# Optimization experiments

Measured on AMD Instinct MI355X. Metric: run time of the kernel, lower is better.

## Reference

```python
import jax, jax.numpy as jnp
import numpy as np

NUM_HEADS = 12
ALPHA = 4.0
EPS = 1e-6

def safe_pow(x, p):
    # relu(x)**p with grad-safe handling of x<=0 (avoids nan from log(0) in pow grads)
    xp = jnp.where(x > 0, x, 1.0)
    return jnp.where(x > 0, xp ** p, 0.0)

def setup_inputs() -> dict:
    key = jax.random.key(0)
    ks = jax.random.split(key, 9)
    B, N, C = 8, 4096, 768
    Hn, hd, ksz = NUM_HEADS, C // NUM_HEADS, 5
    return {
        "x": jax.random.normal(ks[0], (B, N, C), jnp.float32),
        "Wqg": jax.random.normal(ks[1], (C, 2 * C), jnp.float32) * 0.02,
        "Wkv": jax.random.normal(ks[2], (C, 2 * C), jnp.float32) * 0.02,
        "Wproj": jax.random.normal(ks[3], (C, C), jnp.float32) * 0.02,
        "bproj": jnp.zeros((C,), jnp.float32),
        "dwc_w": jax.random.normal(ks[4], (hd, 1, ksz, ksz), jnp.float32) * 0.05,
        "dwc_b": jnp.zeros((hd,), jnp.float32),
        "power_p": jax.random.normal(ks[5], (1, Hn, 1, hd), jnp.float32) * 0.01,
        "scale_p": jax.random.normal(ks[6], (1, 1, C), jnp.float32) * 0.01,
        "pos_enc": jax.random.normal(ks[7], (1, N, C), jnp.float32) * 0.01,
    }

def reference(x, Wqg, Wkv, Wproj, bproj, dwc_w, dwc_b, power_p, scale_p, pos_enc):
    B, N, C = x.shape
    Hn = NUM_HEADS
    hd = C // Hn
    # q/g projection: [B,N,2C] -> q = [...,0,:], g = [...,1,:]
    qg = (x @ Wqg).reshape(B, N, 2, C)
    q, g = qg[:, :, 0], qg[:, :, 1]
    # k/v projection (sr_ratio == 1)
    kvp = x @ Wkv
    k, v = kvp[..., :C], kvp[..., C:]
    k = k + pos_enc
    scale = jax.nn.softplus(scale_p)            # [1,1,C]
    power = 1.0 + ALPHA * jax.nn.sigmoid(power_p)  # [1,Hn,1,hd]
    q = q / scale
    k = k / scale
    # -> [B,Hn,N,hd]
    q = q.reshape(B, N, Hn, hd).transpose(0, 2, 1, 3)
    k = k.reshape(B, N, Hn, hd).transpose(0, 2, 1, 3)
    v = v.reshape(B, N, Hn, hd).transpose(0, 2, 1, 3)
    q_pos = safe_pow(q, power)
    q_neg = safe_pow(-q, power)
    k_pos = safe_pow(k, power)
    k_neg = safe_pow(-k, power)
    q_sim = jnp.concatenate([q_pos, q_neg], -1)  # [B,Hn,N,2hd]
    q_opp = jnp.concatenate([q_neg, q_pos], -1)
    k_cat = jnp.concatenate([k_pos, k_neg], -1)
    v1, v2 = jnp.split(v, 2, axis=-1)            # [B,Hn,N,hd/2]
    n = N
    inv_n = 1.0 / n
    k_mean = k_cat.mean(axis=2, keepdims=True)   # [B,Hn,1,2hd]
    z_sim = 1.0 / (jnp.einsum('bhnk,bhmk->bhnm', q_sim, k_mean) + EPS)  # [B,Hn,N,1]
    kv1 = jnp.einsum('bhnk,bhnv->bhkv', k_cat, v1) * inv_n
    x_sim = jnp.einsum('bhnk,bhkv->bhnv', q_sim, kv1) * z_sim
    z_opp = 1.0 / (jnp.einsum('bhnk,bhmk->bhnm', q_opp, k_mean) + EPS)
    kv2 = jnp.einsum('bhnk,bhnv->bhkv', k_cat, v2) * inv_n
    x_opp = jnp.einsum('bhnk,bhkv->bhnv', q_opp, kv2) * z_opp
    xa = jnp.concatenate([x_sim, x_opp], -1).transpose(0, 2, 1, 3).reshape(B, N, C)
    # depthwise-conv positional branch on v (head-major channel layout)
    Hs = int(np.sqrt(N))
    v_img = v.reshape(B * Hn, Hs, Hs, hd).transpose(0, 3, 1, 2)  # [B*Hn, hd, Hs, Hs]
    v_conv = jax.lax.conv_general_dilated(
        v_img, dwc_w, (1, 1), 'SAME', feature_group_count=hd,
        dimension_numbers=('NCHW', 'OIHW', 'NCHW')) + dwc_b[None, :, None, None]
    v_pos = v_conv.reshape(B, C, N).transpose(0, 2, 1)  # [B,N,C]
    out = (xa + v_pos) * g
    return out @ Wproj + bproj
```

## Files before the change

kernel.cpp:

```cpp
#include <hip/hip_runtime.h>


typedef _Float16 f16;
typedef __attribute__((ext_vector_type(4))) float f32x4;
typedef __attribute__((ext_vector_type(8))) _Float16 f16x8;
typedef __attribute__((ext_vector_type(4))) _Float16 f16x4;

__device__ __forceinline__ void mfma(f32x4& c, f16x8 a, f16x8 b) {
  c = __builtin_amdgcn_mfma_f32_16x16x32_f16(a, b, c, 0, 0, 0);
}

__device__ __forceinline__ void gload_lds16(const f16* g, f16* l) {
  __builtin_amdgcn_global_load_lds(
      (__attribute__((address_space(1))) void*)g,
      (__attribute__((address_space(3))) void*)l, 16, 0, 0);
}

__device__ __forceinline__ f16x8 relu8(f16x8 v) {
  f16x8 r;
#pragma unroll
  for (int u = 0; u < 8; ++u) r[u] = (v[u] > (f16)0) ? v[u] : (f16)0;
  return r;
}
__device__ __forceinline__ f16x8 nrelu8(f16x8 v) {
  f16x8 r;
#pragma unroll
  for (int u = 0; u < 8; ++u) r[u] = (v[u] < (f16)0) ? (f16)(-v[u]) : (f16)0;
  return r;
}

__global__ void prep_scalars_kernel(const float* __restrict__ scale_p,
                                    const float* __restrict__ power_p,
                                    float* __restrict__ iscale,
                                    float* __restrict__ powr) {
  int c = blockIdx.x * 256 + threadIdx.x;
  if (c < 768) {
    float sp = scale_p[c];
    float s = (sp > 20.f) ? sp : log1pf(__expf(sp));
    iscale[c] = 1.f / s;
    powr[c] = 1.f + 4.f / (1.f + __expf(-power_p[c]));
  }
}

__global__ __launch_bounds__(256) void cast_x_kernel(const float* __restrict__ x,
                                                     f16* __restrict__ xblk) {
  __shared__ f16 tile[128 * 72];
  const int kb = blockIdx.x, mt = blockIdx.y, t = threadIdx.x;
  const float* xp = x + (size_t)mt * 128 * 768 + kb * 64;
#pragma unroll
  for (int it = 0; it < 8; ++it) {
    int idx = it * 256 + t;
    int row = idx >> 4, kc4 = (idx & 15) * 4;
    f32x4 v = *(const f32x4*)(xp + (size_t)row * 768 + kc4);
    f16x4 h;
    h[0] = (f16)v[0]; h[1] = (f16)v[1]; h[2] = (f16)v[2]; h[3] = (f16)v[3];
    *(f16x4*)(tile + row * 72 + kc4) = h;
  }
  __syncthreads();
  f16* op = xblk + (size_t)mt * 98304 + kb * 8192;
#pragma unroll
  for (int it = 0; it < 4; ++it) {
    int c = it * 256 + t;
    int kchunk = c >> 7, m = c & 127;
    f16x4 lo = *(const f16x4*)(tile + m * 72 + kchunk * 8);
    f16x4 hi = *(const f16x4*)(tile + m * 72 + kchunk * 8 + 4);
    *(f16x4*)(op + c * 8) = lo;
    *(f16x4*)(op + c * 8 + 4) = hi;
  }
}

__global__ __launch_bounds__(256) void transpose_w_kernel(const float* __restrict__ W,
                                                          f16* __restrict__ outblk,
                                                          int Cc, int col_off) {
  __shared__ float tile[32][33];
  const int c0 = blockIdx.x * 32, r0 = blockIdx.y * 32, t = threadIdx.x;
#pragma unroll
  for (int it = 0; it < 4; ++it) {
    int rr = it * 8 + (t >> 5), cc = t & 31;
    tile[rr][cc] = W[(size_t)(r0 + rr) * Cc + c0 + cc];
  }
  __syncthreads();
  if (t < 128) {
    int cl = t >> 2, rb = t & 3;
    int cg = col_off + c0 + cl;
    int rg = r0 + rb * 8;
    f16x4 v0, v1;
#pragma unroll
    for (int u = 0; u < 4; ++u) v0[u] = (f16)tile[rb * 8 + u][cl];
#pragma unroll
    for (int u = 0; u < 4; ++u) v1[u] = (f16)tile[rb * 8 + 4 + u][cl];
    size_t base = (size_t)(cg >> 7) * 98304 + (size_t)(rg >> 3) * 1024 +
                  (size_t)(cg & 127) * 8;
    *(f16x4*)(outblk + base) = v0;
    *(f16x4*)(outblk + base + 4) = v1;
  }
}

template <int MODE>
__global__ __launch_bounds__(512) void gemm_kernel(
    const f16* __restrict__ Ablk, const f16* __restrict__ Bblk,
    const float* __restrict__ powr, const float* __restrict__ iscale,
    const float* __restrict__ pos_enc, const float* __restrict__ bproj,
    f16* __restrict__ qpow, f16* __restrict__ gbuf, f16* __restrict__ kpow,
    f16* __restrict__ vt, float* __restrict__ outp) {
  constexpr int NW    = (MODE == 0) ? 4 : 2;
  constexpr int MREP  = (MODE == 0) ? 8 : 4;
  constexpr int BCOLT = (MODE == 0) ? 2 : 1;
  constexpr int A_H   = 16384;
  constexpr int STR   = A_H + BCOLT * 8192;
  extern __shared__ f16 smem[];
  const int t = threadIdx.x;
  const int wid = t >> 6, lane = t & 63;
  const int c16 = lane & 15, q = lane >> 4;
  const int mtile = blockIdx.x, ntile = blockIdx.y;
  const int wm = wid / NW, wn = wid % NW;
  const f16* Ap = Ablk + (size_t)mtile * 196608;
  const f16* Bp = Bblk + (size_t)ntile * (BCOLT * 98304);
  const int ahalf = (MODE == 0) ? wm : (wm >> 1);
  const int rbase = (MODE == 0) ? 0 : (wm & 1) * 64;
  const int bhalf = (MODE == 0) ? (wn >> 1) : 0;
  const int cbase = (MODE == 0) ? (wn & 1) * 64 : wn * 64;

  auto STAGE = [&](int buf, int k0) {
    const size_t gk = (size_t)k0 * 128;
#pragma unroll
    for (int h = 0; h < 2; ++h)
#pragma unroll
      for (int r = 0; r < 2; ++r)
        gload_lds16(Ap + h * 98304 + gk + (size_t)(r * 512 + t) * 8,
                    smem + buf * STR + h * 8192 + (r * 512 + wid * 64) * 8);
#pragma unroll
    for (int h = 0; h < BCOLT; ++h)
#pragma unroll
      for (int r = 0; r < 2; ++r)
        gload_lds16(Bp + h * 98304 + gk + (size_t)(r * 512 + t) * 8,
                    smem + buf * STR + A_H + h * 8192 + (r * 512 + wid * 64) * 8);
  };

  f32x4 acc[MREP][4];
#pragma unroll
  for (int i = 0; i < MREP; ++i)
#pragma unroll
    for (int j = 0; j < 4; ++j) acc[i][j] = (f32x4){0.f, 0.f, 0.f, 0.f};

  STAGE(0, 0);
  STAGE(1, 64);
  if constexpr (MODE == 0) asm volatile("s_waitcnt vmcnt(8)");
  else                     asm volatile("s_waitcnt vmcnt(6)");
  __builtin_amdgcn_sched_barrier(0);
  __builtin_amdgcn_s_barrier();
  __builtin_amdgcn_sched_barrier(0);

  for (int j = 0; j < 12; ++j) {
    const int cur = j & 1;
    const f16* A_ = smem + cur * STR + ahalf * 8192;
    const f16* B_ = smem + cur * STR + A_H + bhalf * 8192;
#pragma unroll
    for (int s2 = 0; s2 < 2; ++s2) {
      f16x8 af[MREP], bf[4];
      const int kc = (s2 * 4 + q) * 1024;
#pragma unroll
      for (int mi = 0; mi < MREP; ++mi)
        af[mi] = *(const f16x8*)(A_ + kc + (rbase + mi * 16 + c16) * 8);
#pragma unroll
      for (int ni = 0; ni < 4; ++ni)
        bf[ni] = *(const f16x8*)(B_ + kc + (cbase + ni * 16 + c16) * 8);
      __builtin_amdgcn_s_setprio(1);
#pragma unroll
      for (int mi = 0; mi < MREP; ++mi)
#pragma unroll
        for (int ni = 0; ni < 4; ++ni) mfma(acc[mi][ni], af[mi], bf[ni]);
      __builtin_amdgcn_s_setprio(0);
    }
    if (j < 11) {
      asm volatile("s_waitcnt lgkmcnt(0)");
      __builtin_amdgcn_sched_barrier(0);
      __builtin_amdgcn_s_barrier();
      __builtin_amdgcn_sched_barrier(0);
      if (j < 10) {
        STAGE(cur, (j + 2) * 64);
        if constexpr (MODE == 0) asm volatile("s_waitcnt vmcnt(8)");
        else                     asm volatile("s_waitcnt vmcnt(6)");
      } else {
        asm volatile("s_waitcnt vmcnt(0)");
      }
      __builtin_amdgcn_sched_barrier(0);
      __builtin_amdgcn_s_barrier();
      __builtin_amdgcn_sched_barrier(0);
    }
  }

  if (MODE == 0) {
    const int sec = ntile / 3;
    const int csb = (ntile - sec * 3) * 256;
    const int b = mtile >> 4;
    const int nim0 = (mtile & 15) * 256;
#pragma unroll
    for (int mi = 0; mi < MREP; ++mi) {
      const int nloc = nim0 + wm * 128 + mi * 16 + q * 4;
#pragma unroll
      for (int ni = 0; ni < 4; ++ni) {
        const int cs = csb + wn * 64 + ni * 16 + c16;
        const int h = cs >> 6, d = cs & 63;
        const int bh = b * 12 + h;
        if (sec == 0) {
          const float p = powr[cs], isc = iscale[cs];
          const size_t qb2 = (size_t)bh * 262144 + (size_t)(nloc >> 7) * 8192;
          const int dpo = (d >> 3) * 1024 + (d & 7);
#pragma unroll
          for (int r2 = 0; r2 < 4; ++r2) {
            float val = acc[mi][ni][r2] * isc;
            float av = fabsf(val);
            float e = (av > 0.f) ? exp2f(p * __log2f(av)) : 0.f;
            float s = (val > 0.f) ? e : ((val < 0.f) ? -e : 0.f);
            int mrow = (nloc + r2) & 127;
            qpow[qb2 + mrow * 8 + dpo] = (f16)s;
          }
        } else if (sec == 1) {
#pragma unroll
          for (int r2 = 0; r2 < 4; ++r2)
            gbuf[((size_t)bh * 4096 + nloc + r2) * 64 + d] = (f16)acc[mi][ni][r2];
        } else if (sec == 2) {
          const float p = powr[cs], isc = iscale[cs];
          f16x4 pk;
#pragma unroll
          for (int r2 = 0; r2 < 4; ++r2) {
            int n = nloc + r2;
            float val = (acc[mi][ni][r2] + pos_enc[(size_t)n * 768 + cs]) * isc;
            float av = fabsf(val);
            float e = (av > 0.f) ? exp2f(p * __log2f(av)) : 0.f;
            pk[r2] = (f16)((val > 0.f) ? e : ((val < 0.f) ? -e : 0.f));
          }
          const size_t kb2 =
              (size_t)bh * 262144 + (size_t)(nloc >> 3) * 512 + (nloc & 7);
          *(f16x4*)(kpow + kb2 + (size_t)d * 8) = pk;
        } else {
          f16x4 vv4;
#pragma unroll
          for (int r2 = 0; r2 < 4; ++r2) vv4[r2] = (f16)acc[mi][ni][r2];
          *(f16x4*)(vt + (size_t)(bh * 64 + d) * 4096 + nloc) = vv4;
        }
      }
    }
  } else {
#pragma unroll
    for (int mi = 0; mi < MREP; ++mi) {
      const int tok0 = mtile * 256 + wm * 64 + mi * 16 + q * 4;
#pragma unroll
      for (int ni = 0; ni < 4; ++ni) {
        const int col = ntile * 128 + wn * 64 + ni * 16 + c16;
        const float bb = bproj[col];
#pragma unroll
        for (int r2 = 0; r2 < 4; ++r2)
          outp[(size_t)(tok0 + r2) * 768 + col] = acc[mi][ni][r2] + bb;
      }
    }
  }
}

__global__ __launch_bounds__(256) void kv_kernel(const f16* __restrict__ kpow,
                                                 const f16* __restrict__ vt,
                                                 float* __restrict__ kvp,
                                                 float* __restrict__ ksp) {
  __shared__ f16 Ks[8192];
  __shared__ f16 Vs[4096];
  __shared__ float rp[256], rn[256];
  const int bh = blockIdx.x, split = blockIdx.y, t = threadIdx.x;
  const int wave = t >> 6, lane = t & 63;
  const int c16 = lane & 15, q = lane >> 4;
  const f16* kb = kpow + (size_t)bh * 262144;
  const f16* vb = vt + (size_t)bh * 64 * 4096;
  f32x4 acc[4][2];
#pragma unroll
  for (int i = 0; i < 4; ++i)
#pragma unroll
    for (int j = 0; j < 2; ++j) acc[i][j] = (f32x4){0.f, 0.f, 0.f, 0.f};
  float sp = 0.f, sn = 0.f;

  const int n_beg = split * 1024, n_end = n_beg + 1024;
  for (int n0 = n_beg; n0 < n_end; n0 += 64) {
    f16x8 kr[2], vr[2];
#pragma unroll
    for (int r = 0; r < 2; ++r)
      kr[r] = *(const f16x8*)(kb + (size_t)n0 * 64 + (size_t)(r * 256 + t) * 8);
#pragma unroll
    for (int r = 0; r < 2; ++r) {
      int cc = r * 256 + t;
      int vv = cc >> 3, nc = cc & 7;
      vr[r] = *(const f16x8*)(vb + (size_t)vv * 4096 + n0 + nc * 8);
    }
#pragma unroll
    for (int r = 0; r < 2; ++r)
#pragma unroll
      for (int u = 0; u < 8; ++u) {
        float f = (float)kr[r][u];
        sp += (f > 0.f) ? f : 0.f;
        sn += (f < 0.f) ? -f : 0.f;
      }
    __syncthreads();
#pragma unroll
    for (int r = 0; r < 2; ++r) {
      int cp = r * 256 + t;
      int nch = cp >> 6, d = cp & 63;
      *(f16x8*)(Ks + (size_t)(nch * 1024 + d * 8)) = relu8(kr[r]);
      *(f16x8*)(Ks + (size_t)(nch * 1024 + (d + 64) * 8)) = nrelu8(kr[r]);
    }
#pragma unroll
    for (int r = 0; r < 2; ++r) {
      int cc = r * 256 + t;
      int vv = cc >> 3, nc = cc & 7;
      *(f16x8*)(Vs + (size_t)(nc * 64 + (vv ^ nc)) * 8) = vr[r];
    }
    __syncthreads();
#pragma unroll
    for (int s = 0; s < 2; ++s) {
      f16x8 af[4], bf2[2];
#pragma unroll
      for (int i = 0; i < 4; ++i) {
        int m = i * 16 + c16, nc2 = s * 4 + q;
        af[i] = *(const f16x8*)(Vs + (nc2 * 64 + (m ^ nc2)) * 8);
      }
#pragma unroll
      for (int j = 0; j < 2; ++j)
        bf2[j] = *(const f16x8*)(Ks + ((s * 4 + q) * 128 + wave * 32 + j * 16 + c16) * 8);
#pragma unroll
      for (int i = 0; i < 4; ++i)
#pragma unroll
        for (int j = 0; j < 2; ++j) mfma(acc[i][j], af[i], bf2[j]);
    }
    __syncthreads();
  }
  float* kvb = kvp + (size_t)(bh * 4 + split) * 8192;
#pragma unroll
  for (int i = 0; i < 4; ++i)
#pragma unroll
    for (int j = 0; j < 2; ++j) {
      int kk = wave * 32 + j * 16 + c16;
      int vv0 = i * 16 + q * 4;
#pragma unroll
      for (int r2 = 0; r2 < 4; ++r2)
        kvb[(size_t)(vv0 + r2) * 128 + kk] = acc[i][j][r2];
    }
  rp[t] = sp; rn[t] = sn;
  __syncthreads();
  if (t < 64) {
    float* ko = ksp + (size_t)(bh * 4 + split) * 128;
    ko[t] = rp[t] + rp[t + 64] + rp[t + 128] + rp[t + 192];
    ko[64 + t] = rn[t] + rn[t + 64] + rn[t + 128] + rn[t + 192];
  }
}

__global__ void bx_kernel(const float* __restrict__ kvp,
                          const float* __restrict__ ksp, f16* __restrict__ bxt) {
  const int bh = blockIdx.x, kk = threadIdx.x;
  const float inv_n = 1.f / 4096.f;
  const float* kv0 = kvp + (size_t)bh * 4 * 8192;
  const float* ks0 = ksp + (size_t)bh * 4 * 128;
  f16* ob = bxt + (size_t)bh * 80 * 128;
  for (int nn = 0; nn < 32; ++nn) {
    float v = kv0[nn * 128 + kk] + kv0[8192 + nn * 128 + kk] +
              kv0[16384 + nn * 128 + kk] + kv0[24576 + nn * 128 + kk];
    ob[nn * 128 + kk] = (f16)(v * inv_n);
  }
  const int kx = kk ^ 64;
  for (int nn = 32; nn < 64; ++nn) {
    float v = kv0[nn * 128 + kx] + kv0[8192 + nn * 128 + kx] +
              kv0[16384 + nn * 128 + kx] + kv0[24576 + nn * 128 + kx];
    ob[nn * 128 + kk] = (f16)(v * inv_n);
  }
  float s0 = ks0[kk] + ks0[128 + kk] + ks0[256 + kk] + ks0[384 + kk];
  ob[64 * 128 + kk] = (f16)(s0 * inv_n);
  float s1 = ks0[kx] + ks0[128 + kx] + ks0[256 + kx] + ks0[384 + kx];
  ob[65 * 128 + kk] = (f16)(s1 * inv_n);
  for (int nn = 66; nn < 80; ++nn) ob[nn * 128 + kk] = (f16)0.f;
}

__global__ __launch_bounds__(256) void conv_kernel(const f16* __restrict__ vt,
                                                   const float* __restrict__ w,
                                                   const float* __restrict__ bias,
                                                   f16* __restrict__ vpos) {
  __shared__ float img[68 * 69];
  const int blk = blockIdx.x;
  const int d = blk & 63, bh = blk >> 6;
  const f16* src = vt + (size_t)(bh * 64 + d) * 4096;
  for (int i = threadIdx.x; i < 68 * 68; i += 256) {
    int yy = i / 68, xx = i - yy * 68;
    int y = yy - 2, x = xx - 2;
    float val = 0.f;
    if (((unsigned)y < 64u) && ((unsigned)x < 64u)) val = (float)src[y * 64 + x];
    img[yy * 69 + xx] = val;
  }
  float wr[25];
#pragma unroll
  for (int k = 0; k < 25; ++k) wr[k] = w[d * 25 + k];
  const float bb = bias[d];
  __syncthreads();
  f16* dst = vpos + (size_t)(bh * 64 + d) * 4096;
  for (int g4 = threadIdx.x; g4 < 1024; g4 += 256) {
    int y = g4 >> 4, x4 = (g4 & 15) * 4;
    float o0 = bb, o1 = bb, o2 = bb, o3 = bb;
#pragma unroll
    for (int ky = 0; ky < 5; ++ky) {
      const float* row = img + (y + ky) * 69 + x4;
      float r[8];
#pragma unroll
      for (int u = 0; u < 8; ++u) r[u] = row[u];
#pragma unroll
      for (int kx = 0; kx < 5; ++kx) {
        float wv = wr[ky * 5 + kx];
        o0 += r[kx] * wv;
        o1 += r[kx + 1] * wv;
        o2 += r[kx + 2] * wv;
        o3 += r[kx + 3] * wv;
      }
    }
    f16x4 st;
    st[0] = (f16)o0; st[1] = (f16)o1; st[2] = (f16)o2; st[3] = (f16)o3;
    *(f16x4*)(dst + y * 64 + x4) = st;
  }
}

__global__ __launch_bounds__(256) void xa_kernel(
    const f16* __restrict__ qpow, const f16* __restrict__ bxt,
    const f16* __restrict__ vpos, const f16* __restrict__ gbuf,
    f16* __restrict__ pre) {
  __shared__ f16 Qs[16384];
  __shared__ f16 Ps[64 * 134];
  __shared__ float zs[256];
  const int nb = blockIdx.x, bh = blockIdx.y;
  const int b = bh / 12, h = bh % 12;
  const int t = threadIdx.x;
  const int wave = t >> 6, lane = t & 63;
  const int c16 = lane & 15, q = lane >> 4;
  const f16* qb = qpow + (size_t)bh * 262144 + (size_t)nb * 8192;
  f16x8 qr[4];
#pragma unroll
  for (int r = 0; r < 4; ++r)
    qr[r] = *(const f16x8*)(qb + (size_t)(r * 256 + t) * 8);
#pragma unroll
  for (int r = 0; r < 4; ++r) {
    int c = r * 256 + t;
    int dch = c >> 7, row = c & 127;
    *(f16x8*)(Qs + (size_t)(dch * 1024 + row * 8)) = relu8(qr[r]);
    *(f16x8*)(Qs + (size_t)((dch + 8) * 1024 + row * 8)) = nrelu8(qr[r]);
  }
  {
    const f16* vpb = vpos + (size_t)bh * 262144 + (size_t)nb * 128;
#pragma unroll
    for (int it = 0; it < 4; ++it) {
      int idx = it * 256 + t;
      int col = idx >> 4, nc = idx & 15;
      f16x8 v = *(const f16x8*)(vpb + (size_t)col * 4096 + nc * 8);
      *(f16x8*)(Ps + col * 134 + nc * 8) = v;
    }
  }
  __syncthreads();
  f32x4 acc[2][5];
#pragma unroll
  for (int i = 0; i < 2; ++i)
#pragma unroll
    for (int j = 0; j < 5; ++j) acc[i][j] = (f32x4){0.f, 0.f, 0.f, 0.f};
  const f16* bx = bxt + (size_t)bh * 80 * 128;
#pragma unroll
  for (int s = 0; s < 4; ++s) {
    f16x8 af[2], bf5[5];
#pragma unroll
    for (int i = 0; i < 2; ++i)
      af[i] = *(const f16x8*)(Qs + ((s * 4 + q) * 1024 + (wave * 32 + i * 16 + c16) * 8));
#pragma unroll
    for (int j = 0; j < 5; ++j)
      bf5[j] = *(const f16x8*)(bx + (size_t)(j * 16 + c16) * 128 + s * 32 + q * 8);
#pragma unroll
    for (int i = 0; i < 2; ++i)
#pragma unroll
      for (int j = 0; j < 5; ++j) mfma(acc[i][j], af[i], bf5[j]);
  }
  if (c16 < 2) {
#pragma unroll
    for (int i = 0; i < 2; ++i) {
      int mloc = wave * 32 + i * 16 + q * 4;
#pragma unroll
      for (int r2 = 0; r2 < 4; ++r2) zs[(mloc + r2) * 2 + c16] = acc[i][4][r2];
    }
  }
  __syncthreads();
#pragma unroll
  for (int i = 0; i < 2; ++i) {
    const int mbase = wave * 32 + i * 16 + q * 4;
#pragma unroll
    for (int j = 0; j < 4; ++j) {
      const int col = j * 16 + c16;
      const int cch = h * 64 + col;
      const int zsel = col >> 5;
#pragma unroll
      for (int r2 = 0; r2 < 4; ++r2) {
        const int mloc = mbase + r2;
        const int n = nb * 128 + mloc;
        const float den = zs[mloc * 2 + zsel];
        const float xav = acc[i][j][r2] / (den + 1e-6f);
        const float vp = (float)Ps[col * 134 + mloc];
        const float gg = (float)gbuf[((size_t)bh * 4096 + n) * 64 + col];
        const int tok = b * 4096 + n;
        pre[(size_t)(tok >> 7) * 98304 + (size_t)(cch >> 3) * 1024 +
            (tok & 127) * 8 + (cch & 7)] = (f16)((xav + vp) * gg);
      }
    }
  }
}

extern "C" void kernel_launch(void* const* d_in, const int* in_sizes, int n_in,
                              void* d_out, int out_size, void* d_ws, size_t ws_size,
                              hipStream_t stream) {
  const float* x       = (const float*)d_in[0];
  const float* Wqg     = (const float*)d_in[1];
  const float* Wkv     = (const float*)d_in[2];
  const float* Wproj   = (const float*)d_in[3];
  const float* bproj   = (const float*)d_in[4];
  const float* dwc_w   = (const float*)d_in[5];
  const float* dwc_b   = (const float*)d_in[6];
  const float* power_p = (const float*)d_in[7];
  const float* scale_p = (const float*)d_in[8];
  const float* pos_enc = (const float*)d_in[9];
  float* outp = (float*)d_out;

  char* ws = (char*)d_ws;
  constexpr size_t o_qpow = 0;
  constexpr size_t o_kpow = 50331648;
  constexpr size_t o_vt   = 100663296;
  constexpr size_t o_gbuf = 150994944;
  constexpr size_t o_xblk = 201326592;
  constexpr size_t o_wta  = 251658240;
  constexpr size_t o_wtp  = 256376832;
  constexpr size_t o_isc  = 257556480;
  constexpr size_t o_pwr  = 257560576;
  constexpr size_t o_bxt  = 257564672;

  f16*   qpow = (f16*)(ws + o_qpow);
  f16*   kpow = (f16*)(ws + o_kpow);
  f16*   vt   = (f16*)(ws + o_vt);
  f16*   gbuf = (f16*)(ws + o_gbuf);
  f16*   xblk = (f16*)(ws + o_xblk);
  f16*   wta  = (f16*)(ws + o_wta);
  f16*   wtp  = (f16*)(ws + o_wtp);
  float* isc  = (float*)(ws + o_isc);
  float* pwr  = (float*)(ws + o_pwr);
  f16*   bxt  = (f16*)(ws + o_bxt);
  float* kvp  = (float*)(ws + o_xblk);
  float* ksp  = (float*)(ws + o_xblk + 12582912);
  f16*   vpos = kpow;
  f16*   pre  = xblk;

  prep_scalars_kernel<<<dim3(3), 256, 0, stream>>>(scale_p, power_p, isc, pwr);
  cast_x_kernel<<<dim3(12, 256), 256, 0, stream>>>(x, xblk);
  transpose_w_kernel<<<dim3(48, 24), 256, 0, stream>>>(Wqg, wta, 1536, 0);
  transpose_w_kernel<<<dim3(48, 24), 256, 0, stream>>>(Wkv, wta, 1536, 1536);
  transpose_w_kernel<<<dim3(24, 24), 256, 0, stream>>>(Wproj, wtp, 768, 0);
  gemm_kernel<0><<<dim3(128, 12), 512, 131072, stream>>>(
      xblk, wta, pwr, isc, pos_enc, nullptr, qpow, gbuf, kpow, vt, nullptr);
  kv_kernel<<<dim3(96, 4), 256, 0, stream>>>(kpow, vt, kvp, ksp);
  bx_kernel<<<96, 128, 0, stream>>>(kvp, ksp, bxt);
  conv_kernel<<<6144, 256, 0, stream>>>(vt, dwc_w, dwc_b, vpos);
  xa_kernel<<<dim3(32, 96), 256, 0, stream>>>(qpow, bxt, vpos, gbuf, pre);
  gemm_kernel<1><<<dim3(128, 6), 512, 98304, stream>>>(
      pre, wtp, nullptr, nullptr, nullptr, bproj, nullptr, nullptr, nullptr,
      nullptr, outp);
}
```

Measured before the change: 611.1 us.

## Interleave global-to-LDS prefetch with MFMA phases in GEMM main loop

The GEMM main loop is restructured into finer phases. Each phase issues a slice of the next tiles' global-to-LDS loads between LDS fragment reads and MFMA bursts. Buffer halves are refilled progressively, one row group at a time, instead of as a whole stage after a barrier. The goal is to hide load latency and avoid the stall at the end of each k-step, at the cost of more barriers per iteration and more delicate vmcnt accounting.

After: 635.1 us. 1.04x slower.

```diff
diff --git a/kernel.cpp b/kernel.cpp
--- a/kernel.cpp
+++ b/kernel.cpp
@@ -121,21 +121,14 @@
   const int bhalf = (MODE == 0) ? (wn >> 1) : 0;
   const int cbase = (MODE == 0) ? (wn & 1) * 64 : wn * 64;
 
-  auto STAGE = [&](int buf, int k0) {
-    const size_t gk = (size_t)k0 * 128;
-#pragma unroll
-    for (int h = 0; h < 2; ++h)
-#pragma unroll
-      for (int r = 0; r < 2; ++r)
-        gload_lds16(Ap + h * 98304 + gk + (size_t)(r * 512 + t) * 8,
-                    smem + buf * STR + h * 8192 + (r * 512 + wid * 64) * 8);
-#pragma unroll
-    for (int h = 0; h < BCOLT; ++h)
-#pragma unroll
-      for (int r = 0; r < 2; ++r)
-        gload_lds16(Bp + h * 98304 + gk + (size_t)(r * 512 + t) * 8,
-                    smem + buf * STR + A_H + h * 8192 + (r * 512 + wid * 64) * 8);
+  auto stageA = [&](int buf, int k0, int h, int r) {
+    gload_lds16(Ap + (size_t)h * 98304 + (size_t)k0 * 128 + (size_t)(r * 512 + t) * 8,
+                smem + buf * STR + h * 8192 + (r * 512 + wid * 64) * 8);
   };
+  auto stageB = [&](int buf, int k0, int h, int r) {
+    gload_lds16(Bp + (size_t)h * 98304 + (size_t)k0 * 128 + (size_t)(r * 512 + t) * 8,
+                smem + buf * STR + A_H + h * 8192 + (r * 512 + wid * 64) * 8);
+  };
 
   f32x4 acc[MREP][4];
 #pragma unroll
@@ -143,50 +136,106 @@
 #pragma unroll
     for (int j = 0; j < 4; ++j) acc[i][j] = (f32x4){0.f, 0.f, 0.f, 0.f};
 
-  STAGE(0, 0);
-  STAGE(1, 64);
-  if constexpr (MODE == 0) asm volatile("s_waitcnt vmcnt(8)");
-  else                     asm volatile("s_waitcnt vmcnt(6)");
+  if constexpr (MODE == 0) {
+    stageA(0, 0, 0, 0); stageA(0, 0, 1, 0); stageB(0, 0, 0, 0); stageB(0, 0, 1, 0);
+    stageA(0, 0, 0, 1); stageA(0, 0, 1, 1); stageB(0, 0, 0, 1); stageB(0, 0, 1, 1);
+    stageA(1, 64, 0, 0); stageA(1, 64, 1, 0); stageB(1, 64, 0, 0); stageB(1, 64, 1, 0);
+    asm volatile("s_waitcnt vmcnt(4)");
+  } else {
+    stageA(0, 0, 0, 0); stageA(0, 0, 1, 0); stageB(0, 0, 0, 0);
+    stageA(0, 0, 0, 1); stageA(0, 0, 1, 1); stageB(0, 0, 0, 1);
+    stageA(1, 64, 0, 0); stageA(1, 64, 1, 0); stageB(1, 64, 0, 0);
+    asm volatile("s_waitcnt vmcnt(3)");
+  }
   __builtin_amdgcn_sched_barrier(0);
   __builtin_amdgcn_s_barrier();
   __builtin_amdgcn_sched_barrier(0);
 
-  for (int j = 0; j < 12; ++j) {
-    const int cur = j & 1;
-    const f16* A_ = smem + cur * STR + ahalf * 8192;
-    const f16* B_ = smem + cur * STR + A_H + bhalf * 8192;
-#pragma unroll
-    for (int s2 = 0; s2 < 2; ++s2) {
-      f16x8 af[MREP], bf[4];
-      const int kc = (s2 * 4 + q) * 1024;
-#pragma unroll
-      for (int mi = 0; mi < MREP; ++mi)
-        af[mi] = *(const f16x8*)(A_ + kc + (rbase + mi * 16 + c16) * 8);
-#pragma unroll
-      for (int ni = 0; ni < 4; ++ni)
-        bf[ni] = *(const f16x8*)(B_ + kc + (cbase + ni * 16 + c16) * 8);
-      __builtin_amdgcn_s_setprio(1);
-#pragma unroll
-      for (int mi = 0; mi < MREP; ++mi)
-#pragma unroll
-        for (int ni = 0; ni < 4; ++ni) mfma(acc[mi][ni], af[mi], bf[ni]);
-      __builtin_amdgcn_s_setprio(0);
-    }
-    if (j < 11) {
-      asm volatile("s_waitcnt lgkmcnt(0)");
-      __builtin_amdgcn_sched_barrier(0);
-      __builtin_amdgcn_s_barrier();
-      __builtin_amdgcn_sched_barrier(0);
-      if (j < 10) {
-        STAGE(cur, (j + 2) * 64);
-        if constexpr (MODE == 0) asm volatile("s_waitcnt vmcnt(8)");
-        else                     asm volatile("s_waitcnt vmcnt(6)");
-      } else {
-        asm volatile("s_waitcnt vmcnt(0)");
-      }
-      __builtin_amdgcn_sched_barrier(0);
-      __builtin_amdgcn_s_barrier();
-      __builtin_amdgcn_sched_barrier(0);
+  if constexpr (MODE == 0) {
+    f16x8 bf[4];
+    for (int j = 0; j < 12; ++j) {
+      const int cur = j & 1;
+      const f16* A_ = smem + cur * STR + ahalf * 8192;
+      const f16* B_ = smem + cur * STR + A_H + bhalf * 8192;
+#pragma unroll
+      for (int ph = 0; ph < 4; ++ph) {
+        const int s2 = ph >> 1, mh = ph & 1;
+        const int kc = (s2 * 4 + q) * 1024;
+        f16x8 af[4];
+#pragma unroll
+        for (int mi = 0; mi < 4; ++mi)
+          af[mi] = *(const f16x8*)(A_ + kc + ((mh * 4 + mi) * 16 + c16) * 8);
+        if (mh == 0) {
+#pragma unroll
+          for (int ni = 0; ni < 4; ++ni)
+            bf[ni] = *(const f16x8*)(B_ + kc + (cbase + ni * 16 + c16) * 8);
+        }
+        if (ph == 0 && j < 11) { stageA(cur ^ 1, (j + 1) * 64, 0, 1); stageA(cur ^ 1, (j + 1) * 64, 1, 1); }
+        if (ph == 1 && j < 11) { stageB(cur ^ 1, (j + 1) * 64, 0, 1); stageB(cur ^ 1, (j + 1) * 64, 1, 1); }
+        if (ph == 2 && j < 10) { stageA(cur, (j + 2) * 64, 0, 0); stageA(cur, (j + 2) * 64, 1, 0); }
+        if (ph == 3 && j < 10) { stageB(cur, (j + 2) * 64, 0, 0); stageB(cur, (j + 2) * 64, 1, 0); }
+        __builtin_amdgcn_sched_barrier(0);
+        __builtin_amdgcn_s_barrier();
+        asm volatile("s_waitcnt lgkmcnt(0)");
+        __builtin_amdgcn_sched_barrier(0);
+        __builtin_amdgcn_s_setprio(1);
+#pragma unroll
+        for (int mi = 0; mi < 4; ++mi)
+#pragma unroll
+          for (int ni = 0; ni < 4; ++ni)
+            mfma(acc[mh * 4 + mi][ni], af[mi], bf[ni]);
+        __builtin_amdgcn_s_setprio(0);
+        if (ph == 3) {
+          if (j < 10)       asm volatile("s_waitcnt vmcnt(4)");
+          else if (j == 10) asm volatile("s_waitcnt vmcnt(0)");
+        }
+        __builtin_amdgcn_sched_barrier(0);
+        __builtin_amdgcn_s_barrier();
+        __builtin_amdgcn_sched_barrier(0);
+      }
+    }
+  } else {
+    for (int j = 0; j < 12; ++j) {
+      const int cur = j & 1;
+      const f16* A_ = smem + cur * STR + ahalf * 8192;
+      const f16* B_ = smem + cur * STR + A_H;
+#pragma unroll
+      for (int ph = 0; ph < 2; ++ph) {
+        const int kc = (ph * 4 + q) * 1024;
+        f16x8 af[4], bf[4];
+#pragma unroll
+        for (int mi = 0; mi < 4; ++mi)
+          af[mi] = *(const f16x8*)(A_ + kc + (rbase + mi * 16 + c16) * 8);
+#pragma unroll
+        for (int ni = 0; ni < 4; ++ni)
+          bf[ni] = *(const f16x8*)(B_ + kc + (cbase + ni * 16 + c16) * 8);
+        if (ph == 0 && j < 11) {
+          stageA(cur ^ 1, (j + 1) * 64, 0, 1); stageA(cur ^ 1, (j + 1) * 64, 1, 1);
+          stageB(cur ^ 1, (j + 1) * 64, 0, 1);
+        }
+        if (ph == 1 && j < 10) {
+          stageA(cur, (j + 2) * 64, 0, 0); stageA(cur, (j + 2) * 64, 1, 0);
+          stageB(cur, (j + 2) * 64, 0, 0);
+        }
+        __builtin_amdgcn_sched_barrier(0);
+        __builtin_amdgcn_s_barrier();
+        asm volatile("s_waitcnt lgkmcnt(0)");
+        __builtin_amdgcn_sched_barrier(0);
+        __builtin_amdgcn_s_setprio(1);
+#pragma unroll
+        for (int mi = 0; mi < 4; ++mi)
+#pragma unroll
+          for (int ni = 0; ni < 4; ++ni)
+            mfma(acc[mi][ni], af[mi], bf[ni]);
+        __builtin_amdgcn_s_setprio(0);
+        if (ph == 1) {
+          if (j < 10)       asm volatile("s_waitcnt vmcnt(3)");
+          else if (j == 10) asm volatile("s_waitcnt vmcnt(0)");
+        }
+        __builtin_amdgcn_sched_barrier(0);
+        __builtin_amdgcn_s_barrier();
+        __builtin_amdgcn_sched_barrier(0);
+      }
     }
   }
 
```

## Shrink GEMM tiles to 128x256 with smaller K-steps for higher occupancy

Applied to the files above, without the earlier changes.

Both GEMM instantiations now use one 128x256 tile with a 32-wide K step, static 48KB LDS double buffer, and launch bounds requesting 4 blocks per CU. The prefetch of the next stage is issued before compute of the current one, with a single barrier per iteration. The grid is swapped so N tiles index x, improving A-tile reuse across neighbouring blocks. The aim is more resident waves to hide latency. The cost is less register reuse per block and more barriers over 24 K iterations.

Result: no change. 617.0 us (+1.0%).

```diff
diff --git a/kernel.cpp b/kernel.cpp
--- a/kernel.cpp
+++ b/kernel.cpp
@@ -97,107 +97,80 @@
 }
 
 template <int MODE>
-__global__ __launch_bounds__(512) void gemm_kernel(
+__global__ __launch_bounds__(512, 4) void gemm_kernel(
     const f16* __restrict__ Ablk, const f16* __restrict__ Bblk,
     const float* __restrict__ powr, const float* __restrict__ iscale,
     const float* __restrict__ pos_enc, const float* __restrict__ bproj,
     f16* __restrict__ qpow, f16* __restrict__ gbuf, f16* __restrict__ kpow,
     f16* __restrict__ vt, float* __restrict__ outp) {
-  constexpr int NW    = (MODE == 0) ? 4 : 2;
-  constexpr int MREP  = (MODE == 0) ? 8 : 4;
-  constexpr int BCOLT = (MODE == 0) ? 2 : 1;
-  constexpr int A_H   = 16384;
-  constexpr int STR   = A_H + BCOLT * 8192;
-  extern __shared__ f16 smem[];
+  constexpr int A_SZ = 4096;
+  constexpr int STR  = 12288;
+  __shared__ f16 smem[2 * STR];
   const int t = threadIdx.x;
   const int wid = t >> 6, lane = t & 63;
   const int c16 = lane & 15, q = lane >> 4;
-  const int mtile = blockIdx.x, ntile = blockIdx.y;
-  const int wm = wid / NW, wn = wid % NW;
-  const f16* Ap = Ablk + (size_t)mtile * 196608;
-  const f16* Bp = Bblk + (size_t)ntile * (BCOLT * 98304);
-  const int ahalf = (MODE == 0) ? wm : (wm >> 1);
-  const int rbase = (MODE == 0) ? 0 : (wm & 1) * 64;
-  const int bhalf = (MODE == 0) ? (wn >> 1) : 0;
-  const int cbase = (MODE == 0) ? (wn & 1) * 64 : wn * 64;
+  const int ntile = blockIdx.x, mtile = blockIdx.y;
+  const int wm = wid >> 2, wn = wid & 3;
+  const int bh2 = wn >> 1, bc = (wn & 1) * 64;
+  const f16* Ap = Ablk + (size_t)mtile * 98304;
+  const f16* Bp = Bblk + (size_t)ntile * 196608;
 
   auto STAGE = [&](int buf, int k0) {
-    const size_t gk = (size_t)k0 * 128;
-#pragma unroll
-    for (int h = 0; h < 2; ++h)
-#pragma unroll
-      for (int r = 0; r < 2; ++r)
-        gload_lds16(Ap + h * 98304 + gk + (size_t)(r * 512 + t) * 8,
-                    smem + buf * STR + h * 8192 + (r * 512 + wid * 64) * 8);
-#pragma unroll
-    for (int h = 0; h < BCOLT; ++h)
-#pragma unroll
-      for (int r = 0; r < 2; ++r)
-        gload_lds16(Bp + h * 98304 + gk + (size_t)(r * 512 + t) * 8,
-                    smem + buf * STR + A_H + h * 8192 + (r * 512 + wid * 64) * 8);
+    const size_t gk = (size_t)(k0 >> 3) * 1024;
+    gload_lds16(Ap + gk + (size_t)t * 8, smem + buf * STR + wid * 512);
+    gload_lds16(Bp + gk + (size_t)t * 8, smem + buf * STR + A_SZ + wid * 512);
+    gload_lds16(Bp + 98304 + gk + (size_t)t * 8,
+                smem + buf * STR + A_SZ + 4096 + wid * 512);
   };
 
-  f32x4 acc[MREP][4];
-#pragma unroll
-  for (int i = 0; i < MREP; ++i)
+  f32x4 acc[4][4];
+#pragma unroll
+  for (int i = 0; i < 4; ++i)
 #pragma unroll
     for (int j = 0; j < 4; ++j) acc[i][j] = (f32x4){0.f, 0.f, 0.f, 0.f};
 
   STAGE(0, 0);
-  STAGE(1, 64);
-  if constexpr (MODE == 0) asm volatile("s_waitcnt vmcnt(8)");
-  else                     asm volatile("s_waitcnt vmcnt(6)");
+  asm volatile("s_waitcnt vmcnt(0)");
   __builtin_amdgcn_sched_barrier(0);
   __builtin_amdgcn_s_barrier();
   __builtin_amdgcn_sched_barrier(0);
 
-  for (int j = 0; j < 12; ++j) {
+  for (int j = 0; j < 24; ++j) {
     const int cur = j & 1;
-    const f16* A_ = smem + cur * STR + ahalf * 8192;
-    const f16* B_ = smem + cur * STR + A_H + bhalf * 8192;
-#pragma unroll
-    for (int s2 = 0; s2 < 2; ++s2) {
-      f16x8 af[MREP], bf[4];
-      const int kc = (s2 * 4 + q) * 1024;
-#pragma unroll
-      for (int mi = 0; mi < MREP; ++mi)
-        af[mi] = *(const f16x8*)(A_ + kc + (rbase + mi * 16 + c16) * 8);
-#pragma unroll
-      for (int ni = 0; ni < 4; ++ni)
-        bf[ni] = *(const f16x8*)(B_ + kc + (cbase + ni * 16 + c16) * 8);
-      __builtin_amdgcn_s_setprio(1);
-#pragma unroll
-      for (int mi = 0; mi < MREP; ++mi)
-#pragma unroll
-        for (int ni = 0; ni < 4; ++ni) mfma(acc[mi][ni], af[mi], bf[ni]);
-      __builtin_amdgcn_s_setprio(0);
-    }
-    if (j < 11) {
-      asm volatile("s_waitcnt lgkmcnt(0)");
-      __builtin_amdgcn_sched_barrier(0);
-      __builtin_amdgcn_s_barrier();
-      __builtin_amdgcn_sched_barrier(0);
-      if (j < 10) {
-        STAGE(cur, (j + 2) * 64);
-        if constexpr (MODE == 0) asm volatile("s_waitcnt vmcnt(8)");
-        else                     asm volatile("s_waitcnt vmcnt(6)");
-      } else {
-        asm volatile("s_waitcnt vmcnt(0)");
-      }
-      __builtin_amdgcn_sched_barrier(0);
-      __builtin_amdgcn_s_barrier();
-      __builtin_amdgcn_sched_barrier(0);
-    }
+    if (j < 23) STAGE(cur ^ 1, (j + 1) * 32);
+    const f16* A_ = smem + cur * STR;
+    const f16* B_ = smem + cur * STR + A_SZ + bh2 * 4096;
+    f16x8 af[4], bf[4];
+    const int kc = q * 1024;
+#pragma unroll
+    for (int mi = 0; mi < 4; ++mi)
+      af[mi] = *(const f16x8*)(A_ + kc + (wm * 64 + mi * 16 + c16) * 8);
+#pragma unroll
+    for (int ni = 0; ni < 4; ++ni)
+      bf[ni] = *(const f16x8*)(B_ + kc + (bc + ni * 16 + c16) * 8);
+    asm volatile("s_waitcnt lgkmcnt(0)");
+    __builtin_amdgcn_sched_barrier(0);
+    __builtin_amdgcn_s_setprio(1);
+#pragma unroll
+    for (int mi = 0; mi < 4; ++mi)
+#pragma unroll
+      for (int ni = 0; ni < 4; ++ni) mfma(acc[mi][ni], af[mi], bf[ni]);
+    __builtin_amdgcn_s_setprio(0);
+    __builtin_amdgcn_sched_barrier(0);
+    if (j < 23) asm volatile("s_waitcnt vmcnt(0)");
+    __builtin_amdgcn_sched_barrier(0);
+    __builtin_amdgcn_s_barrier();
+    __builtin_amdgcn_sched_barrier(0);
   }
 
   if (MODE == 0) {
     const int sec = ntile / 3;
     const int csb = (ntile - sec * 3) * 256;
-    const int b = mtile >> 4;
-    const int nim0 = (mtile & 15) * 256;
-#pragma unroll
-    for (int mi = 0; mi < MREP; ++mi) {
-      const int nloc = nim0 + wm * 128 + mi * 16 + q * 4;
+    const int b = mtile >> 5;
+    const int nim0 = (mtile & 31) * 128;
+#pragma unroll
+    for (int mi = 0; mi < 4; ++mi) {
+      const int nloc = nim0 + wm * 64 + mi * 16 + q * 4;
 #pragma unroll
       for (int ni = 0; ni < 4; ++ni) {
         const int cs = csb + wn * 64 + ni * 16 + c16;
@@ -244,11 +217,11 @@
     }
   } else {
 #pragma unroll
-    for (int mi = 0; mi < MREP; ++mi) {
-      const int tok0 = mtile * 256 + wm * 64 + mi * 16 + q * 4;
+    for (int mi = 0; mi < 4; ++mi) {
+      const int tok0 = mtile * 128 + wm * 64 + mi * 16 + q * 4;
 #pragma unroll
       for (int ni = 0; ni < 4; ++ni) {
-        const int col = ntile * 128 + wn * 64 + ni * 16 + c16;
+        const int col = ntile * 256 + wn * 64 + ni * 16 + c16;
         const float bb = bproj[col];
 #pragma unroll
         for (int r2 = 0; r2 < 4; ++r2)
@@ -555,13 +528,13 @@
   transpose_w_kernel<<<dim3(48, 24), 256, 0, stream>>>(Wqg, wta, 1536, 0);
   transpose_w_kernel<<<dim3(48, 24), 256, 0, stream>>>(Wkv, wta, 1536, 1536);
   transpose_w_kernel<<<dim3(24, 24), 256, 0, stream>>>(Wproj, wtp, 768, 0);
-  gemm_kernel<0><<<dim3(128, 12), 512, 131072, stream>>>(
+  gemm_kernel<0><<<dim3(12, 256), 512, 0, stream>>>(
       xblk, wta, pwr, isc, pos_enc, nullptr, qpow, gbuf, kpow, vt, nullptr);
   kv_kernel<<<dim3(96, 4), 256, 0, stream>>>(kpow, vt, kvp, ksp);
   bx_kernel<<<96, 128, 0, stream>>>(kvp, ksp, bxt);
   conv_kernel<<<6144, 256, 0, stream>>>(vt, dwc_w, dwc_b, vpos);
   xa_kernel<<<dim3(32, 96), 256, 0, stream>>>(qpow, bxt, vpos, gbuf, pre);
-  gemm_kernel<1><<<dim3(128, 6), 512, 98304, stream>>>(
+  gemm_kernel<1><<<dim3(3, 256), 512, 0, stream>>>(
       pre, wtp, nullptr, nullptr, nullptr, bproj, nullptr, nullptr, nullptr,
       nullptr, outp);
 }
```
